# Optimization experiments

Hardware: AMD Instinct MI355X
Metric: run time of the kernel (lower is better)

## Reference

```python
import jax, jax.numpy as jnp
import numpy as np
from jax import lax
from jax.scipy.special import logsumexp

KX = jnp.array([[1., 0., -1.], [2., 0., -2.], [1., 0., -1.]], jnp.float32).reshape(1, 1, 3, 3)
KY = jnp.array([[1., 2., 1.], [0., 0., 0.], [-1., -2., -1.]], jnp.float32).reshape(1, 1, 3, 3)
SINK_EPS = 0.05 ** 2  # geomloss SamplesLoss('sinkhorn', p=2, blur=0.05): eps = blur**p
SINK_ITERS = 10
N_SUB = 4096


def _gauss1d(size, sigma):
    x = jnp.arange(size, dtype=jnp.float32) - (size - 1) / 2.0
    k = jnp.exp(-(x * x) / (2.0 * sigma * sigma))
    return k / k.sum()


def _sep_filter(x, k, sym_pad):
    # separable 2D filter; x [B,C,H,W], k [ks]. VALID conv; optional symmetric pad (scipy 'reflect').
    B, C, H, W = x.shape
    xr = x.reshape(B * C, 1, H, W)
    if sym_pad:
        r = k.shape[0] // 2
        xr = jnp.pad(xr, ((0, 0), (0, 0), (r, r), (r, r)), mode='symmetric')
    o = lax.conv_general_dilated(xr, k.reshape(1, 1, -1, 1), (1, 1), 'VALID')
    o = lax.conv_general_dilated(o, k.reshape(1, 1, 1, -1), (1, 1), 'VALID')
    return o.reshape(B, C, o.shape[2], o.shape[3])


def _ssim_per_sample(x, y):
    # standard gaussian-window SSIM (11x11, sigma=1.5, data_range=1.0), mean per sample -> [B]
    k = _gauss1d(11, 1.5)
    mu1, mu2 = _sep_filter(x, k, False), _sep_filter(y, k, False)
    s11 = _sep_filter(x * x, k, False) - mu1 * mu1
    s22 = _sep_filter(y * y, k, False) - mu2 * mu2
    s12 = _sep_filter(x * y, k, False) - mu1 * mu2
    C1, C2 = 0.01 ** 2, 0.03 ** 2
    m = ((2 * mu1 * mu2 + C1) * (2 * s12 + C2)) / ((mu1 * mu1 + mu2 * mu2 + C1) * (s11 + s22 + C2))
    return m.mean(axis=(1, 2, 3))


def _sobel(x):
    # SobelGrad.forward: per-channel magnitude, per-(b,c) max-normalized, channel-mean -> [B,1,H,W]
    B, C, H, W = x.shape
    xr = x.reshape(B * C, 1, H, W)
    gx = lax.conv_general_dilated(xr, KX, (1, 1), ((1, 1), (1, 1)))
    gy = lax.conv_general_dilated(xr, KY, (1, 1), ((1, 1), (1, 1)))
    mag = jnp.sqrt(gx * gx + gy * gy + 1e-6).reshape(B, C, H, W)
    mag = mag / jnp.maximum(mag.max(axis=(2, 3), keepdims=True), 1e-6)
    return mag.mean(1, keepdims=True)


def _avgpool2(x):
    B, C, H, W = x.shape
    return x.reshape(B, C, H // 2, 2, W // 2, 2).mean(axis=(3, 5))


def _charb_mean(d):
    return jnp.sqrt(d * d + 1e-6).mean()  # charbonnier eps=1e-3


def _ot_eps(x, y):
    # entropic OT value with uniform weights, log-domain Sinkhorn, envelope gradient (geomloss-style:
    # iterations detached, one differentiable update at the end).
    N, M = x.shape[0], y.shape[0]
    C = 0.5 * (jnp.sum(x * x, 1)[:, None] + jnp.sum(y * y, 1)[None, :] - 2.0 * x @ y.T)  # p=2 cost |x-y|^2/2
    Cd = lax.stop_gradient(C)
    loga, logb = -float(np.log(N)), -float(np.log(M))
    def body(carry, _):
        f, g = carry
        g = -SINK_EPS * logsumexp(loga + (f[:, None] - Cd) / SINK_EPS, axis=0)
        f = -SINK_EPS * logsumexp(logb + (g[None, :] - Cd) / SINK_EPS, axis=1)
        return (f, g), None
    (f, g), _ = lax.scan(body, (jnp.zeros((N,), x.dtype), jnp.zeros((M,), x.dtype)), None, length=SINK_ITERS)
    f = lax.stop_gradient(f)
    g = -SINK_EPS * logsumexp(loga + (f[:, None] - C) / SINK_EPS, axis=0)
    f = -SINK_EPS * logsumexp(logb + (g[None, :] - C) / SINK_EPS, axis=1)
    return f.mean() + g.mean()


def _sinkhorn_div(x, y):
    return _ot_eps(x, y) - 0.5 * _ot_eps(x, x) - 0.5 * _ot_eps(y, y)


def _forward(y, mri, pet, mask, ehat, idx):
    B, C, H, W = y.shape
    y_gray = y.mean(1, keepdims=True)
    ssim_m = 1.0 - _ssim_per_sample(y_gray, mri).mean()
    ssim_p = 1.0 - _ssim_per_sample(y, pet).mean()
    g_cons = (_charb_mean(_sobel(y_gray) - _sobel(mri))
              + _charb_mean(_sobel(_avgpool2(y).mean(1, keepdims=True)) - _sobel(_avgpool2(mri))))
    aux = jnp.abs(ehat - lax.stop_gradient(_sobel(mri))).mean()
    # per-sample masked point clouds, fixed 4096-point subsample (idx ~ randperm[:4096])
    y_pts = (y * mask).reshape(B, C, H * W).transpose(0, 2, 1)    # [B,HW,3]
    pet_pts = (pet * mask).reshape(B, C, H * W).transpose(0, 2, 1)
    y_s = jnp.take_along_axis(y_pts, idx[..., None], axis=1)      # [B,4096,3]
    pet_s = jnp.take_along_axis(pet_pts, idx[..., None], axis=1)
    include = ((mask.reshape(B, -1) > 0.1).sum(1) >= 32).astype(y.dtype)  # 'continue' guard
    L_transport = (include * jax.vmap(_sinkhorn_div)(y_s, pet_s)).sum() / B
    L_out = (include * ((y * (1.0 - mask)) ** 2).mean(axis=(1, 2, 3))).sum() / B
    mri_rgb = jnp.broadcast_to(mri, y.shape)
    L_ssim = (include * (1.0 - _ssim_per_sample(y * mask, mri_rgb * mask))).sum() / B
    loss_transport = 0.8 * L_transport + 0.3 * L_out + 0.5 * L_ssim  # alpha, beta, gamma
    L_intensity = 2.5 * jnp.mean((y * mask - pet * mask) ** 2)
    # gaussian_smooth: scipy gaussian_filter sigma=1, truncate=4 -> radius 4, mode 'reflect';
    # torch path detaches before smoothing -> stop_gradient
    smoothed = lax.stop_gradient(_sep_filter(y, _gauss1d(9, 1.0), True))
    L_smooth = jnp.mean((smoothed - y) ** 2)
    total = loss_transport + L_intensity + 0.2 * L_smooth
    return total, ssim_m, ssim_p, g_cons, aux


def setup_inputs() -> dict:
    key = jax.random.key(0)
    ks = jax.random.split(key, 5)
    B, C, H, W = 2, 3, 256, 256
    y = jax.random.uniform(ks[0], (B, C, H, W), jnp.float32)
    mri = jax.random.uniform(ks[1], (B, 1, H, W), jnp.float32)
    pet = jax.random.uniform(ks[2], (B, C, H, W), jnp.float32)
    mask = jax.random.uniform(ks[3], (B, 1, H, W), jnp.float32)
    ehat = jax.random.uniform(ks[4], (B, 1, H, W), jnp.float32)
    rng = np.random.default_rng(0)
    idx = jnp.asarray(np.stack([rng.permutation(H * W)[:N_SUB] for _ in range(B)]), dtype=jnp.int32)
    return {"y": y, "mri": mri, "pet": pet, "mask": mask, "ehat": ehat, "idx": idx}


def reference(y, mri, pet, mask, ehat, idx):
    return _forward(y, mri, pet, mask, ehat, idx)
```

## Files before the change

kernel.cpp:

```cpp
#include <hip/hip_runtime.h>
#include <math.h>

#define INV_EPS_L2E 577.0780163555854f
#define EPS_LOGN 0.02079441542f
#define EPS_LN2 0.00173286795f

#define NPTS 4096
#define CHUNK 64
#define NCH 64
#define CPT 8
#define COLS_PER_BLK 2048
#define NCB 2
#define QSTRIDE (NCH * NPTS)

typedef float v2f __attribute__((ext_vector_type(2)));

__device__ __forceinline__ v2f pk_add(v2f a, v2f b) {
    v2f d;
    asm("v_pk_add_f32 %0, %1, %2" : "=v"(d) : "v"(a), "v"(b));
    return d;
}
__device__ __forceinline__ v2f pk_fma_blo(v2f a, v2f b, v2f c) {
    v2f d;
    asm("v_pk_fma_f32 %0, %1, %2, %3 op_sel:[0,0,0] op_sel_hi:[0,1,1]"
        : "=v"(d) : "v"(a), "v"(b), "v"(c));
    return d;
}
__device__ __forceinline__ v2f pk_fma_bhi(v2f a, v2f b, v2f c) {
    v2f d;
    asm("v_pk_fma_f32 %0, %1, %2, %3 op_sel:[1,0,0] op_sel_hi:[1,1,1]"
        : "=v"(d) : "v"(a), "v"(b), "v"(c));
    return d;
}
__device__ __forceinline__ v2f pk_fma_blo_chi(v2f a, v2f b, v2f c) {
    v2f d;
    asm("v_pk_fma_f32 %0, %1, %2, %3 op_sel:[0,0,1] op_sel_hi:[0,1,1]"
        : "=v"(d) : "v"(a), "v"(b), "v"(c));
    return d;
}
__device__ __forceinline__ v2f pk_add_bhi(v2f a, v2f b) {
    v2f d;
    asm("v_pk_add_f32 %0, %1, %2 op_sel:[0,1] op_sel_hi:[1,1]"
        : "=v"(d) : "v"(a), "v"(b));
    return d;
}

constexpr int A_SSIMA  = 0;
constexpr int A_SSIMB  = 2;
constexpr int A_SSIMC  = 4;
constexpr int A_CH1    = 6;
constexpr int A_CH2    = 7;
constexpr int A_AUX    = 8;
constexpr int A_INT    = 9;
constexpr int A_LOUT   = 10;
constexpr int A_CNT    = 12;
constexpr int A_SMOOTH = 14;
constexpr int A_SINK   = 16;
constexpr int A_MAX    = 32;
constexpr int A_DONE   = 40;

__device__ __forceinline__ float blockSum(float v, int tid) {
#pragma unroll
    for (int o = 32; o; o >>= 1) v += __shfl_down(v, o, 64);
    __shared__ float sh[4];
    __syncthreads();
    if ((tid & 63) == 0) sh[tid >> 6] = v;
    __syncthreads();
    return sh[0] + sh[1] + sh[2] + sh[3];
}

__device__ __forceinline__ float blockMax(float v, int tid) {
#pragma unroll
    for (int o = 32; o; o >>= 1) v = fmaxf(v, __shfl_down(v, o, 64));
    __shared__ float sh[4];
    __syncthreads();
    if ((tid & 63) == 0) sh[tid >> 6] = v;
    __syncthreads();
    return fmaxf(fmaxf(sh[0], sh[1]), fmaxf(sh[2], sh[3]));
}

__global__ __launch_bounds__(256) void egf_prep_pool(const float* __restrict__ y,
                                                     const float* __restrict__ pet,
                                                     const float* __restrict__ mri,
                                                     const float* __restrict__ mask,
                                                     const int* __restrict__ idx,
                                                     float* __restrict__ ygray,
                                                     float* __restrict__ py,
                                                     float* __restrict__ pmri,
                                                     float4* __restrict__ pts,
                                                     float* __restrict__ acc) {
    int b = blockIdx.y;
    int x = blockIdx.x;
    if (x < 64) {
        float inten = 0.0f, lout = 0.0f, cnt = 0.0f;
#pragma unroll
        for (int k = 0; k < 4; k++) {
            int p = x * 1024 + k * 256 + threadIdx.x;
            float m  = mask[b * 65536 + p];
            float y0 = y[(b * 3 + 0) * 65536 + p];
            float y1 = y[(b * 3 + 1) * 65536 + p];
            float y2 = y[(b * 3 + 2) * 65536 + p];
            float q0 = pet[(b * 3 + 0) * 65536 + p];
            float q1 = pet[(b * 3 + 1) * 65536 + p];
            float q2 = pet[(b * 3 + 2) * 65536 + p];
            ygray[b * 65536 + p] = (y0 + y1 + y2) * (1.0f / 3.0f);
            float d0 = m * y0 - m * q0, d1 = m * y1 - m * q1, d2 = m * y2 - m * q2;
            inten += d0 * d0 + d1 * d1 + d2 * d2;
            float im = 1.0f - m;
            float o0 = y0 * im, o1 = y1 * im, o2 = y2 * im;
            lout += o0 * o0 + o1 * o1 + o2 * o2;
            cnt += (m > 0.1f) ? 1.0f : 0.0f;
        }
        float t;
        t = blockSum(inten, threadIdx.x); if (threadIdx.x == 0) atomicAdd(&acc[A_INT], t);
        t = blockSum(lout,  threadIdx.x); if (threadIdx.x == 0) atomicAdd(&acc[A_LOUT + b], t);
        t = blockSum(cnt,   threadIdx.x); if (threadIdx.x == 0) atomicAdd(&acc[A_CNT + b], t);
    } else if (x < 80) {
#pragma unroll
        for (int k = 0; k < 4; k++) {
            int po = (x - 64) * 1024 + k * 256 + threadIdx.x;
            int i = po >> 7, j = po & 127;
            int p0 = (i * 2) * 256 + j * 2;
            float s = 0.0f;
#pragma unroll
            for (int c = 0; c < 3; c++) {
                const float* ip = y + (b * 3 + c) * 65536;
                s += ip[p0] + ip[p0 + 1] + ip[p0 + 256] + ip[p0 + 257];
            }
            py[b * 16384 + po] = s * (1.0f / 12.0f);
            const float* mp = mri + b * 65536;
            pmri[b * 16384 + po] = (mp[p0] + mp[p0 + 1] + mp[p0 + 256] + mp[p0 + 257]) * 0.25f;
        }
    } else {
#pragma unroll
        for (int k = 0; k < 4; k++) {
            int t = (b * 4 + (x - 80)) * 1024 + k * 256 + threadIdx.x;
            int bb = t >> 12, j = t & 4095;
            int p = idx[bb * 4096 + j];
            float m = mask[bb * 65536 + p];
            float a0 = y[(bb * 3 + 0) * 65536 + p] * m;
            float a1 = y[(bb * 3 + 1) * 65536 + p] * m;
            float a2 = y[(bb * 3 + 2) * 65536 + p] * m;
            pts[(bb * 2 + 0) * 4096 + j] = make_float4(a0, a1, a2, 0.5f * (a0 * a0 + a1 * a1 + a2 * a2));
            float c0 = pet[(bb * 3 + 0) * 65536 + p] * m;
            float c1 = pet[(bb * 3 + 1) * 65536 + p] * m;
            float c2 = pet[(bb * 3 + 2) * 65536 + p] * m;
            pts[(bb * 2 + 1) * 4096 + j] = make_float4(c0, c1, c2, 0.5f * (c0 * c0 + c1 * c1 + c2 * c2));
        }
    }
}

__global__ __launch_bounds__(256) void egf_sobel4(const float* __restrict__ yg,
                                                  const float* __restrict__ mri,
                                                  const float* __restrict__ py,
                                                  const float* __restrict__ pmri,
                                                  float* __restrict__ mag_yg,
                                                  float* __restrict__ mag_mri,
                                                  float* __restrict__ mag_py,
                                                  float* __restrict__ mag_pmri,
                                                  unsigned* __restrict__ mx) {
    int b = blockIdx.y;
    int x = blockIdx.x;
    const float* in; float* mag; int H, logH, slot, p0;
    if (x < 64)       { in = yg;   mag = mag_yg;   H = 256; logH = 8; slot = 0; p0 = x * 1024; }
    else if (x < 128) { in = mri;  mag = mag_mri;  H = 256; logH = 8; slot = 2; p0 = (x - 64) * 1024; }
    else if (x < 144) { in = py;   mag = mag_py;   H = 128; logH = 7; slot = 4; p0 = (x - 128) * 1024; }
    else              { in = pmri; mag = mag_pmri; H = 128; logH = 7; slot = 6; p0 = (x - 144) * 1024; }
    int HH = H * H;
    const float* ip = in + b * HH;
    float bm = 0.0f;
#pragma unroll
    for (int k = 0; k < 4; k++) {
        int p = p0 + k * 256 + threadIdx.x;
        int i = p >> logH, j = p & (H - 1);
        auto at = [&](int ii, int jj) -> float {
            return (ii >= 0 && ii < H && jj >= 0 && jj < H) ? ip[(ii << logH) + jj] : 0.0f;
        };
        float a00 = at(i - 1, j - 1), a01 = at(i - 1, j), a02 = at(i - 1, j + 1);
        float a10 = at(i, j - 1),                         a12 = at(i, j + 1);
        float a20 = at(i + 1, j - 1), a21 = at(i + 1, j), a22 = at(i + 1, j + 1);
        float gx = a00 - a02 + 2.0f * a10 - 2.0f * a12 + a20 - a22;
        float gy = a00 + 2.0f * a01 + a02 - a20 - 2.0f * a21 - a22;
        float m = sqrtf(gx * gx + gy * gy + 1e-6f);
        mag[b * HH + p] = m;
        bm = fmaxf(bm, m);
    }
    float bmax = blockMax(bm, threadIdx.x);
    if (threadIdx.x == 0) atomicMax(mx + slot + b, __float_as_uint(bmax));
}

__global__ __launch_bounds__(256) void egf_charb2(const float* __restrict__ mag_yg,
                                                  const float* __restrict__ mag_mri,
                                                  const float* __restrict__ mag_py,
                                                  const float* __restrict__ mag_pmri,
                                                  const unsigned* __restrict__ mx,
                                                  const float* __restrict__ ehat,
                                                  float* __restrict__ acc) {
    int b = blockIdx.y;
    int x = blockIdx.x;
    const float *magA, *magB; const unsigned *mxA, *mxB;
    float *accC; const float* eh; int HH, p0;
    if (x < 64) { magA = mag_yg; magB = mag_mri; mxA = mx + 0; mxB = mx + 2;
                  accC = acc + A_CH1; eh = ehat; HH = 65536; p0 = x * 1024; }
    else        { magA = mag_py; magB = mag_pmri; mxA = mx + 4; mxB = mx + 6;
                  accC = acc + A_CH2; eh = nullptr; HH = 16384; p0 = (x - 64) * 1024; }
    float da = fmaxf(__uint_as_float(mxA[b]), 1e-6f);
    float db = fmaxf(__uint_as_float(mxB[b]), 1e-6f);
    float ida = 1.0f / da, idb = 1.0f / db;
    float c = 0.0f, au = 0.0f;
#pragma unroll
    for (int k = 0; k < 4; k++) {
        int p = p0 + k * 256 + threadIdx.x;
        float sa = magA[b * HH + p] * ida;
        float sb = magB[b * HH + p] * idb;
        float d = sa - sb;
        c += sqrtf(d * d + 1e-6f);
        if (eh) au += fabsf(eh[b * HH + p] - sb);
    }
    float tc = blockSum(c, threadIdx.x);
    if (threadIdx.x == 0) atomicAdd(accC, tc);
    if (eh) {
        float ta = blockSum(au, threadIdx.x);
        if (threadIdx.x == 0) atomicAdd(&acc[A_AUX], ta);
    }
}

__global__ __launch_bounds__(256) void egf_ssim3(const float* __restrict__ y,
                                                 const float* __restrict__ ygray,
                                                 const float* __restrict__ mri,
                                                 const float* __restrict__ pet,
                                                 const float* __restrict__ mask,
                                                 float* __restrict__ acc) {
    int z = blockIdx.z;
    const float *xp, *yp, *mp = nullptr; float* accB; int b;
    if (z < 2) {
        b = z; xp = ygray + b * 65536; yp = mri + b * 65536; accB = acc + A_SSIMA;
    } else if (z < 8) {
        int bc = z - 2; b = bc / 3; int c = bc - b * 3;
        xp = y + (b * 3 + c) * 65536; yp = pet + (b * 3 + c) * 65536; accB = acc + A_SSIMB;
    } else {
        int bc = z - 8; b = bc / 3; int c = bc - b * 3;
        xp = y + (b * 3 + c) * 65536; yp = mri + b * 65536; mp = mask + b * 65536; accB = acc + A_SSIMC;
    }
    __shared__ float sx[26][27];
    __shared__ float sy[26][27];
    __shared__ float va[16][27];
    __shared__ float vb[16][27];
    __shared__ float vc[16][27];
    __shared__ float vd[16][27];
    __shared__ float ve[16][27];
    int tid = threadIdx.y * 16 + threadIdx.x;
    float w[11];
    {
        float s = 0.0f;
#pragma unroll
        for (int i = 0; i < 11; i++) { float d = (float)(i - 5); w[i] = expf(-d * d * (1.0f / 4.5f)); s += w[i]; }
        float inv = 1.0f / s;
#pragma unroll
        for (int i = 0; i < 11; i++) w[i] *= inv;
    }
    float vsum = 0.0f;
    for (int st = 0; st < 4; ++st) {
        int ti = (blockIdx.x * 2 + (st >> 1)) * 16;
        int tj = (blockIdx.y * 2 + (st & 1)) * 16;
        for (int t = tid; t < 26 * 26; t += 256) {
            int li = t / 26, lj = t - li * 26;
            int gi = ti + li, gj = tj + lj;
            float a = 0.0f, bb = 0.0f;
            if (gi < 256 && gj < 256) {
                int p = (gi << 8) + gj;
                float m = mp ? mp[p] : 1.0f;
                a = xp[p] * m; bb = yp[p] * m;
            }
            sx[li][lj] = a; sy[li][lj] = bb;
        }
        __syncthreads();
        for (int t = tid; t < 16 * 26; t += 256) {
            int r = t / 26, c = t - r * 26;
            float s0 = 0, s1 = 0, s2 = 0, s3 = 0, s4 = 0;
#pragma unroll
            for (int k = 0; k < 11; k++) {
                float wk = w[k];
                float a = sx[r + k][c], bb = sy[r + k][c];
                s0 += wk * a; s1 += wk * bb;
                s2 += wk * a * a; s3 += wk * bb * bb; s4 += wk * a * bb;
            }
            va[r][c] = s0; vb[r][c] = s1; vc[r][c] = s2; vd[r][c] = s3; ve[r][c] = s4;
        }
        __syncthreads();
        int oi = ti + threadIdx.y, oj = tj + threadIdx.x;
        if (oi < 246 && oj < 246) {
            float mu1 = 0, mu2 = 0, xx = 0, yy = 0, xy = 0;
            int ty = threadIdx.y, tx = threadIdx.x;
#pragma unroll
            for (int k = 0; k < 11; k++) {
                float wk = w[k];
                mu1 += wk * va[ty][tx + k]; mu2 += wk * vb[ty][tx + k];
                xx  += wk * vc[ty][tx + k]; yy  += wk * vd[ty][tx + k];
                xy  += wk * ve[ty][tx + k];
            }
            float s11 = xx - mu1 * mu1, s22 = yy - mu2 * mu2, s12 = xy - mu1 * mu2;
            const float C1 = 1e-4f, C2 = 9e-4f;
            vsum += ((2.0f * mu1 * mu2 + C1) * (2.0f * s12 + C2)) /
                    ((mu1 * mu1 + mu2 * mu2 + C1) * (s11 + s22 + C2));
        }
        __syncthreads();
    }
    float tot = blockSum(vsum, tid);
    if (tid == 0) atomicAdd(&accB[b], tot);
}

__device__ __forceinline__ int refl256(int i) { return i < 0 ? -1 - i : (i > 255 ? 511 - i : i); }

__device__ __forceinline__ void gauss9(float* w) {
    float s = 0.0f;
#pragma unroll
    for (int t = 0; t < 9; t++) { float d = (float)(t - 4); w[t] = expf(-0.5f * d * d); s += w[t]; }
    float inv = 1.0f / s;
#pragma unroll
    for (int t = 0; t < 9; t++) w[t] *= inv;
}

__global__ __launch_bounds__(256) void egf_smooth1(const float* __restrict__ y,
                                                   float* __restrict__ acc) {
    int bc = blockIdx.z;
    const float* ip = y + bc * 65536;
    __shared__ float sx[24][25];
    __shared__ float sv[16][25];
    int tid = threadIdx.x;
    float w[9]; gauss9(w);
    float dsum = 0.0f;
    for (int st = 0; st < 4; ++st) {
        int i0 = (blockIdx.x * 2 + (st >> 1)) * 16;
        int j0 = (blockIdx.y * 2 + (st & 1)) * 16;
        __syncthreads();
        for (int t = tid; t < 576; t += 256) {
            int li = t / 24, lj = t - li * 24;
            int gi = refl256(i0 + li - 4), gj = refl256(j0 + lj - 4);
            sx[li][lj] = ip[(gi << 8) + gj];
        }
        __syncthreads();
        for (int t = tid; t < 384; t += 256) {
            int li = t / 24, lj = t - li * 24;
            float s = 0.0f;
#pragma unroll
            for (int k = 0; k < 9; k++) s += w[k] * sx[li + k][lj];
            sv[li][lj] = s;
        }
        __syncthreads();
        int ty = tid >> 4, tx = tid & 15;
        float s = 0.0f;
#pragma unroll
        for (int k = 0; k < 9; k++) s += w[k] * sv[ty][tx + k];
        float d = s - sx[ty + 4][tx + 4];
        dsum += d * d;
    }
    float tt = blockSum(dsum, tid);
    if (tid == 0) atomicAdd(acc, tt);
}

__device__ __forceinline__ float stageCombine(const float* __restrict__ Pin,
                                              int qbase, int row, int h, int r_local,
                                              float* sm, float* ss, int tid) {
    const float* p = Pin + qbase + (h * 16) * NPTS + row;
    float t[16];
#pragma unroll
    for (int k = 0; k < 16; k++) t[k] = p[k * NPTS];
    float m16 = -3.4e38f;
#pragma unroll
    for (int k = 0; k < 16; k++) m16 = fmaxf(m16, t[k]);
    float s16 = 0.0f;
#pragma unroll
    for (int k = 0; k < 16; k++) s16 += __builtin_amdgcn_exp2f(t[k] - m16);
    sm[h * 64 + r_local] = m16;
    ss[h * 64 + r_local] = s16;
    __syncthreads();
    float v = 0.0f;
    if (tid < 64) {
        float m0 = sm[tid], m1 = sm[64 + tid], m2 = sm[128 + tid], m3 = sm[192 + tid];
        float M = fmaxf(fmaxf(m0, m1), fmaxf(m2, m3));
        float S = ss[tid]       * __builtin_amdgcn_exp2f(m0 - M) +
                  ss[64 + tid]  * __builtin_amdgcn_exp2f(m1 - M) +
                  ss[128 + tid] * __builtin_amdgcn_exp2f(m2 - M) +
                  ss[192 + tid] * __builtin_amdgcn_exp2f(m3 - M);
        v = EPS_LOGN - EPS_LN2 * (M + log2f(S));
    }
    return v;
}

__global__ __launch_bounds__(256) void egf_sink_half8(const float4* __restrict__ pts,
                                                      const float* __restrict__ Pin,
                                                      float* __restrict__ Pout,
                                                      int dir, int init) {
    int q = blockIdx.z; int b = q / 3, t = q - b * 3;
    int xsel = (t == 2) ? 1 : 0;
    int ysel = (t == 1) ? 0 : 1;
    const float4* rowP = pts + (b * 2 + (dir ? ysel : xsel)) * NPTS;
    const float4* colP = pts + (b * 2 + (dir ? xsel : ysel)) * NPTS;

    __shared__ float4 srow[CHUNK];
    __shared__ float sm[256], ss[256];
    int tid = threadIdx.x;
    int chunk = blockIdx.y;
    int r_local = tid & 63, h = tid >> 6;
    int row = chunk * CHUNK + r_local;

    int col0 = blockIdx.x * COLS_PER_BLK + tid;
    float4 cf[8];
#pragma unroll
    for (int k = 0; k < 8; k++) cf[k] = colP[col0 + k * 256];

    float v = 0.0f;
    if (!init)
        v = stageCombine(Pin, q * QSTRIDE, row, h, r_local, sm, ss, tid);
    if (tid < 64) {
        float4 pp = rowP[row];
        srow[tid] = make_float4(pp.x * INV_EPS_L2E, pp.y * INV_EPS_L2E,
                                pp.z * INV_EPS_L2E, (v - pp.w) * INV_EPS_L2E);
    }
    __syncthreads();

    v2f cx[4], cy[4], cz[4], cw[4];
#pragma unroll
    for (int p = 0; p < 4; p++) {
        cx[p] = (v2f){cf[2 * p].x, cf[2 * p + 1].x};
        cy[p] = (v2f){cf[2 * p].y, cf[2 * p + 1].y};
        cz[p] = (v2f){cf[2 * p].z, cf[2 * p + 1].z};
        cw[p] = (v2f){cf[2 * p].w * INV_EPS_L2E, cf[2 * p + 1].w * INV_EPS_L2E};
    }
    v2f mx[4];
#pragma unroll
    for (int p = 0; p < 4; p++) mx[p] = (v2f){-3.4e38f, -3.4e38f};
#pragma unroll 4
    for (int rr = 0; rr < CHUNK; rr++) {
        float4 rp = srow[rr];
        v2f rxy = (v2f){rp.x, rp.y};
        v2f rzw = (v2f){rp.z, rp.w};
#pragma unroll
        for (int p = 0; p < 4; p++) {
            v2f e = pk_fma_blo_chi(rzw, cz[p], rzw);
            e = pk_fma_bhi(rxy, cy[p], e);
            e = pk_fma_blo(rxy, cx[p], e);
            mx[p].x = fmaxf(mx[p].x, e.x);
            mx[p].y = fmaxf(mx[p].y, e.y);
        }
    }
    v2f mneg[4], sa[4];
#pragma unroll
    for (int p = 0; p < 4; p++) { mneg[p] = -mx[p]; sa[p] = (v2f){0.0f, 0.0f}; }
#pragma unroll 4
    for (int rr = 0; rr < CHUNK; rr++) {
        float4 rp = srow[rr];
        v2f rxy = (v2f){rp.x, rp.y};
        v2f rzw = (v2f){rp.z, rp.w};
#pragma unroll
        for (int p = 0; p < 4; p++) {
            v2f e = pk_fma_blo(rzw, cz[p], mneg[p]);
            e = pk_fma_bhi(rxy, cy[p], e);
            e = pk_fma_blo(rxy, cx[p], e);
            e = pk_add_bhi(e, rzw);
            v2f ex;
            ex.x = __builtin_amdgcn_exp2f(e.x);
            ex.y = __builtin_amdgcn_exp2f(e.y);
            sa[p] = pk_add(sa[p], ex);
        }
    }
    float* om = Pout + q * QSTRIDE + chunk * NPTS;
#pragma unroll
    for (int p = 0; p < 4; p++) {
        om[col0 + (2 * p) * 256]     = mx[p].x - cw[p].x + log2f(sa[p].x);
        om[col0 + (2 * p + 1) * 256] = mx[p].y - cw[p].y + log2f(sa[p].y);
    }
}

__device__ __forceinline__ void finalize_body(float* acc, float* out) {
    auto rd = [&](int i) -> float { return atomicAdd(&acc[i], 0.0f); };
    const float AREA = 246.0f * 246.0f;
    float ssim_m = 1.0f - (rd(A_SSIMA) + rd(A_SSIMA + 1)) / (2.0f * AREA);
    float ssim_p = 1.0f - (rd(A_SSIMB) + rd(A_SSIMB + 1)) / (2.0f * 3.0f * AREA);
    float g_cons = rd(A_CH1) / (2.0f * 65536.0f) + rd(A_CH2) / (2.0f * 16384.0f);
    float aux = rd(A_AUX) / (2.0f * 65536.0f);
    float inc0 = (rd(A_CNT)     >= 31.5f) ? 1.0f : 0.0f;
    float inc1 = (rd(A_CNT + 1) >= 31.5f) ? 1.0f : 0.0f;
    float v0 = rd(A_SINK + 0), v1 = rd(A_SINK + 1), v2 = rd(A_SINK + 2);
    float v3 = rd(A_SINK + 3), v4 = rd(A_SINK + 4), v5 = rd(A_SINK + 5);
    float Lt = (inc0 * (v0 - 0.5f * v1 - 0.5f * v2) +
                inc1 * (v3 - 0.5f * v4 - 0.5f * v5)) * 0.5f;
    float Lo = (inc0 * rd(A_LOUT) + inc1 * rd(A_LOUT + 1)) / (3.0f * 65536.0f) * 0.5f;
    float Ls = (inc0 * (1.0f - rd(A_SSIMC) / (3.0f * AREA)) +
                inc1 * (1.0f - rd(A_SSIMC + 1) / (3.0f * AREA))) * 0.5f;
    float Li = 2.5f * rd(A_INT) / (2.0f * 3.0f * 65536.0f);
    float Lsm = rd(A_SMOOTH) / (2.0f * 3.0f * 65536.0f);
    float total = 0.8f * Lt + 0.3f * Lo + 0.5f * Ls + Li + 0.2f * Lsm;
    out[0] = total; out[1] = ssim_m; out[2] = ssim_p; out[3] = g_cons; out[4] = aux;
}

__global__ __launch_bounds__(256) void egf_sink_val8(const float* __restrict__ Pf,
                                                     const float* __restrict__ Pg,
                                                     float* __restrict__ acc,
                                                     float* __restrict__ out) {
    int q = blockIdx.y;
    int side = blockIdx.x >> 6;
    int chunk = blockIdx.x & 63;
    const float* P = side ? Pg : Pf;
    __shared__ float sm[256], ss[256];
    int tid = threadIdx.x;
    int r_local = tid & 63, h = tid >> 6;
    int row = chunk * CHUNK + r_local;
    float v = stageCombine(P, q * QSTRIDE, row, h, r_local, sm, ss, tid);
    float tot = blockSum(v, tid);
    if (tid == 0) {
        atomicAdd(&acc[A_SINK + q], tot * (1.0f / 4096.0f));
        __threadfence();
        unsigned old = atomicAdd((unsigned*)&acc[A_DONE], 1u);
        if (old == 128u * 6u - 1u) finalize_body(acc, out);
    }
}

extern "C" void kernel_launch(void* const* d_in, const int* in_sizes, int n_in,
                              void* d_out, int out_size, void* d_ws, size_t ws_size,
                              hipStream_t stream) {
    const float* y    = (const float*)d_in[0];
    const float* mri  = (const float*)d_in[1];
    const float* pet  = (const float*)d_in[2];
    const float* mask = (const float*)d_in[3];
    const float* ehat = (const float*)d_in[4];
    const int*   idx  = (const int*)d_in[5];
    float* out = (float*)d_out;
    float* ws  = (float*)d_ws;

    float* acc   = ws;
    float4* pts  = (float4*)(ws + 64);
    float* base  = ws + 64 + 65536;

    float* Pf = base;
    float* Pg = Pf + QSTRIDE * 6;
    float* ibase = base + 2 * QSTRIDE * 6;

    float* ygray    = ibase;
    float* py       = ygray + 131072;
    float* pmri     = py + 32768;
    float* mag_yg   = pmri + 32768;
    float* mag_mri  = mag_yg + 131072;
    float* mag_py   = mag_mri + 131072;
    float* mag_pmri = mag_py + 32768;

    hipMemsetAsync(acc, 0, 64 * sizeof(float), stream);

    unsigned* mx = (unsigned*)(acc + A_MAX);

    egf_prep_pool<<<dim3(84, 2), 256, 0, stream>>>(y, pet, mri, mask, idx,
                                                   ygray, py, pmri, pts, acc);
    egf_sobel4<<<dim3(160, 2), 256, 0, stream>>>(ygray, mri, py, pmri,
                                                 mag_yg, mag_mri, mag_py, mag_pmri, mx);
    egf_charb2<<<dim3(80, 2), 256, 0, stream>>>(mag_yg, mag_mri, mag_py, mag_pmri, mx, ehat, acc);
    egf_ssim3<<<dim3(8, 8, 14), dim3(16, 16), 0, stream>>>(y, ygray, mri, pet, mask, acc);
    egf_smooth1<<<dim3(8, 8, 6), 256, 0, stream>>>(y, acc + A_SMOOTH);

    dim3 sgrid(NCB, NCH, 6);
    for (int it = 0; it < 11; ++it) {
        egf_sink_half8<<<sgrid, 256, 0, stream>>>(pts, Pf, Pg, 0, it == 0 ? 1 : 0);
        egf_sink_half8<<<sgrid, 256, 0, stream>>>(pts, Pg, Pf, 1, 0);
    }
    egf_sink_val8<<<dim3(128, 6), 256, 0, stream>>>(Pf, Pg, acc, out);
}
```

Baseline: 719.5 us.

## Fold SSIM and smoothing work into Sinkhorn half-iteration launches as extra blocks

Removes the separate SSIM and Gaussian-smooth kernel launches and spreads their 1280 tile blocks, 128 per launch, across the first ten Sinkhorn half-iteration launches using an extra grid z-slice. The aim is to fill idle CUs in the small 768-block Sinkhorn grids and drop two launches. Shared memory is unified into one buffer sized for the largest user. This raises shared-memory use for the Sinkhorn blocks, which could lower occupancy, and the auxiliary blocks may lengthen the critical path of each Sinkhorn iteration.

```diff
diff --git a/kernel.cpp b/kernel.cpp
--- a/kernel.cpp
+++ b/kernel.cpp
@@ -225,31 +225,29 @@
     }
 }
 
-__global__ __launch_bounds__(256) void egf_ssim3(const float* __restrict__ y,
-                                                 const float* __restrict__ ygray,
-                                                 const float* __restrict__ mri,
-                                                 const float* __restrict__ pet,
-                                                 const float* __restrict__ mask,
-                                                 float* __restrict__ acc) {
-    int z = blockIdx.z;
+__device__ void ssim_dev(int a, int tid, float* smem,
+                         const float* __restrict__ y, const float* __restrict__ ygray,
+                         const float* __restrict__ mri, const float* __restrict__ pet,
+                         const float* __restrict__ mask, float* __restrict__ acc) {
+    int bx = a & 7, by = (a >> 3) & 7, bz = a >> 6;
+    int tx = tid & 15, ty = tid >> 4;
     const float *xp, *yp, *mp = nullptr; float* accB; int b;
-    if (z < 2) {
-        b = z; xp = ygray + b * 65536; yp = mri + b * 65536; accB = acc + A_SSIMA;
-    } else if (z < 8) {
-        int bc = z - 2; b = bc / 3; int c = bc - b * 3;
+    if (bz < 2) {
+        b = bz; xp = ygray + b * 65536; yp = mri + b * 65536; accB = acc + A_SSIMA;
+    } else if (bz < 8) {
+        int bc = bz - 2; b = bc / 3; int c = bc - b * 3;
         xp = y + (b * 3 + c) * 65536; yp = pet + (b * 3 + c) * 65536; accB = acc + A_SSIMB;
     } else {
-        int bc = z - 8; b = bc / 3; int c = bc - b * 3;
+        int bc = bz - 8; b = bc / 3; int c = bc - b * 3;
         xp = y + (b * 3 + c) * 65536; yp = mri + b * 65536; mp = mask + b * 65536; accB = acc + A_SSIMC;
     }
-    __shared__ float sx[26][27];
-    __shared__ float sy[26][27];
-    __shared__ float va[16][27];
-    __shared__ float vb[16][27];
-    __shared__ float vc[16][27];
-    __shared__ float vd[16][27];
-    __shared__ float ve[16][27];
-    int tid = threadIdx.y * 16 + threadIdx.x;
+    float (*sx)[27] = (float(*)[27])(smem);
+    float (*sy)[27] = (float(*)[27])(smem + 702);
+    float (*va)[27] = (float(*)[27])(smem + 1404);
+    float (*vb)[27] = (float(*)[27])(smem + 1836);
+    float (*vc)[27] = (float(*)[27])(smem + 2268);
+    float (*vd)[27] = (float(*)[27])(smem + 2700);
+    float (*ve)[27] = (float(*)[27])(smem + 3132);
     float w[11];
     {
         float s = 0.0f;
@@ -261,18 +259,18 @@
     }
     float vsum = 0.0f;
     for (int st = 0; st < 4; ++st) {
-        int ti = (blockIdx.x * 2 + (st >> 1)) * 16;
-        int tj = (blockIdx.y * 2 + (st & 1)) * 16;
+        int ti = (bx * 2 + (st >> 1)) * 16;
+        int tj = (by * 2 + (st & 1)) * 16;
         for (int t = tid; t < 26 * 26; t += 256) {
             int li = t / 26, lj = t - li * 26;
             int gi = ti + li, gj = tj + lj;
-            float a = 0.0f, bb = 0.0f;
+            float aa = 0.0f, bb = 0.0f;
             if (gi < 256 && gj < 256) {
                 int p = (gi << 8) + gj;
                 float m = mp ? mp[p] : 1.0f;
-                a = xp[p] * m; bb = yp[p] * m;
+                aa = xp[p] * m; bb = yp[p] * m;
             }
-            sx[li][lj] = a; sy[li][lj] = bb;
+            sx[li][lj] = aa; sy[li][lj] = bb;
         }
         __syncthreads();
         for (int t = tid; t < 16 * 26; t += 256) {
@@ -281,17 +279,16 @@
 #pragma unroll
             for (int k = 0; k < 11; k++) {
                 float wk = w[k];
-                float a = sx[r + k][c], bb = sy[r + k][c];
-                s0 += wk * a; s1 += wk * bb;
-                s2 += wk * a * a; s3 += wk * bb * bb; s4 += wk * a * bb;
+                float aa = sx[r + k][c], bb = sy[r + k][c];
+                s0 += wk * aa; s1 += wk * bb;
+                s2 += wk * aa * aa; s3 += wk * bb * bb; s4 += wk * aa * bb;
             }
             va[r][c] = s0; vb[r][c] = s1; vc[r][c] = s2; vd[r][c] = s3; ve[r][c] = s4;
         }
         __syncthreads();
-        int oi = ti + threadIdx.y, oj = tj + threadIdx.x;
+        int oi = ti + ty, oj = tj + tx;
         if (oi < 246 && oj < 246) {
             float mu1 = 0, mu2 = 0, xx = 0, yy = 0, xy = 0;
-            int ty = threadIdx.y, tx = threadIdx.x;
 #pragma unroll
             for (int k = 0; k < 11; k++) {
                 float wk = w[k];
@@ -312,27 +309,25 @@
 
 __device__ __forceinline__ int refl256(int i) { return i < 0 ? -1 - i : (i > 255 ? 511 - i : i); }
 
-__device__ __forceinline__ void gauss9(float* w) {
-    float s = 0.0f;
-#pragma unroll
-    for (int t = 0; t < 9; t++) { float d = (float)(t - 4); w[t] = expf(-0.5f * d * d); s += w[t]; }
-    float inv = 1.0f / s;
-#pragma unroll
-    for (int t = 0; t < 9; t++) w[t] *= inv;
-}
-
-__global__ __launch_bounds__(256) void egf_smooth1(const float* __restrict__ y,
-                                                   float* __restrict__ acc) {
-    int bc = blockIdx.z;
+__device__ void smooth_dev(int a, int tid, float* smem,
+                           const float* __restrict__ y, float* __restrict__ acc) {
+    int bx = a & 7, by = (a >> 3) & 7, bc = a >> 6;
     const float* ip = y + bc * 65536;
-    __shared__ float sx[24][25];
-    __shared__ float sv[16][25];
-    int tid = threadIdx.x;
-    float w[9]; gauss9(w);
+    float (*sx)[25] = (float(*)[25])(smem);
+    float (*sv)[25] = (float(*)[25])(smem + 600);
+    float w[9];
+    {
+        float s = 0.0f;
+#pragma unroll
+        for (int t = 0; t < 9; t++) { float d = (float)(t - 4); w[t] = expf(-0.5f * d * d); s += w[t]; }
+        float inv = 1.0f / s;
+#pragma unroll
+        for (int t = 0; t < 9; t++) w[t] *= inv;
+    }
     float dsum = 0.0f;
     for (int st = 0; st < 4; ++st) {
-        int i0 = (blockIdx.x * 2 + (st >> 1)) * 16;
-        int j0 = (blockIdx.y * 2 + (st & 1)) * 16;
+        int i0 = (bx * 2 + (st >> 1)) * 16;
+        int j0 = (by * 2 + (st & 1)) * 16;
         __syncthreads();
         for (int t = tid; t < 576; t += 256) {
             int li = t / 24, lj = t - li * 24;
@@ -391,16 +386,30 @@
 __global__ __launch_bounds__(256) void egf_sink_half8(const float4* __restrict__ pts,
                                                       const float* __restrict__ Pin,
                                                       float* __restrict__ Pout,
-                                                      int dir, int init) {
+                                                      int dir, int init, int aux_base,
+                                                      const float* __restrict__ y,
+                                                      const float* __restrict__ ygray,
+                                                      const float* __restrict__ mri,
+                                                      const float* __restrict__ pet,
+                                                      const float* __restrict__ mask,
+                                                      float* __restrict__ acc) {
+    __shared__ __align__(16) float smem[3564];
+    int tid = threadIdx.x;
+    if (blockIdx.z == 6) {
+        int a = aux_base + (int)blockIdx.x * 64 + (int)blockIdx.y;
+        if (a < 896) ssim_dev(a, tid, smem, y, ygray, mri, pet, mask, acc);
+        else if (a < 1280) smooth_dev(a - 896, tid, smem, y, acc + A_SMOOTH);
+        return;
+    }
     int q = blockIdx.z; int b = q / 3, t = q - b * 3;
     int xsel = (t == 2) ? 1 : 0;
     int ysel = (t == 1) ? 0 : 1;
     const float4* rowP = pts + (b * 2 + (dir ? ysel : xsel)) * NPTS;
     const float4* colP = pts + (b * 2 + (dir ? xsel : ysel)) * NPTS;
 
-    __shared__ float4 srow[CHUNK];
-    __shared__ float sm[256], ss[256];
-    int tid = threadIdx.x;
+    float4* srow = (float4*)smem;
+    float* sm = smem + 256;
+    float* ss = smem + 512;
     int chunk = blockIdx.y;
     int r_local = tid & 63, h = tid >> 6;
     int row = chunk * CHUNK + r_local;
@@ -554,13 +563,19 @@
     egf_sobel4<<<dim3(160, 2), 256, 0, stream>>>(ygray, mri, py, pmri,
                                                  mag_yg, mag_mri, mag_py, mag_pmri, mx);
     egf_charb2<<<dim3(80, 2), 256, 0, stream>>>(mag_yg, mag_mri, mag_py, mag_pmri, mx, ehat, acc);
-    egf_ssim3<<<dim3(8, 8, 14), dim3(16, 16), 0, stream>>>(y, ygray, mri, pet, mask, acc);
-    egf_smooth1<<<dim3(8, 8, 6), 256, 0, stream>>>(y, acc + A_SMOOTH);
-
-    dim3 sgrid(NCB, NCH, 6);
+
+    dim3 sgrid7(NCB, NCH, 7);
+    dim3 sgrid6(NCB, NCH, 6);
+    int ab = 0;
     for (int it = 0; it < 11; ++it) {
-        egf_sink_half8<<<sgrid, 256, 0, stream>>>(pts, Pf, Pg, 0, it == 0 ? 1 : 0);
-        egf_sink_half8<<<sgrid, 256, 0, stream>>>(pts, Pg, Pf, 1, 0);
+        bool a0 = ab < 1280;
+        egf_sink_half8<<<a0 ? sgrid7 : sgrid6, 256, 0, stream>>>(
+            pts, Pf, Pg, 0, it == 0 ? 1 : 0, ab, y, ygray, mri, pet, mask, acc);
+        if (a0) ab += 128;
+        bool a1 = ab < 1280;
+        egf_sink_half8<<<a1 ? sgrid7 : sgrid6, 256, 0, stream>>>(
+            pts, Pg, Pf, 1, 0, ab, y, ygray, mri, pet, mask, acc);
+        if (a1) ab += 128;
     }
     egf_sink_val8<<<dim3(128, 6), 256, 0, stream>>>(Pf, Pg, acc, out);
 }
```

Result: no change. 722.2 us (+0.4%).
